# Kernel tuning notes

Measured on AMD Instinct MI355X. Metric: run time of the kernel, lower is better.

The kernel has to match this reference:

```python
import jax, jax.numpy as jnp
import numpy as np

IMAGE_SIZE = 256
PSIZE = 8
STRIDE = 4
WINDOW = IMAGE_SIZE + 1 - PSIZE  # 249


def _build_indices():
    # replicate image2patch.__init__ mask construction
    cur = np.arange(0, WINDOW, STRIDE)
    if cur[-1] != WINDOW - 1:
        cur = np.append(cur, WINDOW - 1)
    grid = np.arange(WINDOW * WINDOW).reshape(WINDOW, WINDOW)
    mask = grid[np.ix_(cur, cur)].reshape(-1)  # [M] window-origin flat indices
    rows = mask // WINDOW  # [M] patch top-left row
    cols = mask % WINDOW   # [M] patch top-left col
    k = np.arange(PSIZE * PSIZE)
    di, dj = k // PSIZE, k % PSIZE  # offsets within patch; flat index k = i*PSIZE + j
    r_full = rows[:, None] + di[None, :]  # [M, PSIZE^2]
    c_full = cols[:, None] + dj[None, :]  # [M, PSIZE^2]
    return jnp.asarray(r_full, dtype=jnp.int32), jnp.asarray(c_full, dtype=jnp.int32)

R_IDX, C_IDX = _build_indices()


def setup_inputs() -> dict:
    key = jax.random.key(0)
    x = jax.random.normal(key, (32, 8, IMAGE_SIZE, IMAGE_SIZE), dtype=jnp.float32)
    return {"input_data": x}


def reference(input_data):
    # output[b*c, m, i*PSIZE+j] = input_data[b, c, rows[m]+i, cols[m]+j]
    B, C, H, W = input_data.shape
    x = input_data.reshape(B * C, H, W)
    out = x[:, R_IDX, C_IDX]  # [B*C, M, PSIZE^2] vectorized sliding-window gather
    return out
```

## Files before the change

kernel.cpp:

```cpp
#include <hip/hip_runtime.h>


constexpr unsigned NPDIM   = 63;
constexpr unsigned PATCHES = NPDIM * NPDIM;
constexpr unsigned CHUNKS  = 16;
constexpr unsigned NIMG    = 256;

__global__ __launch_bounds__(256) void image2patch_kernel(
    const float4* __restrict__ in4, float4* __restrict__ out4) {
    unsigned gid = blockIdx.x * 256u + threadIdx.x;

    unsigned k4 = gid & 15u;
    unsigned pn = gid >> 4;
    unsigned n  = pn / PATCHES;
    unsigned p  = pn - n * PATCHES;
    unsigned pr = p / NPDIM;
    unsigned pc = p - pr * NPDIM;

    unsigned row  = pr * 4u + (k4 >> 1);
    unsigned col4 = pc + (k4 & 1u);

    out4[gid] = in4[n * 16384u + row * 64u + col4];
}

extern "C" void kernel_launch(void* const* d_in, const int* in_sizes, int n_in,
                              void* d_out, int out_size, void* d_ws, size_t ws_size,
                              hipStream_t stream) {
    const float4* in4 = (const float4*)d_in[0];
    float4* out4 = (float4*)d_out;
    unsigned total4 = NIMG * PATCHES * CHUNKS;
    unsigned blocks = total4 / 256u;
    image2patch_kernel<<<blocks, 256, 0, stream>>>(in4, out4);
}
```

Baseline: 298.5 us.

## Stage patch-row input strip in LDS and emit patches per block

Each block now handles one patch row of one image. It loads the 8x256 input strip into shared memory once, with padded rows to limit bank conflicts, then writes all 63 patches from LDS. This replaces redundant global gathers, where each input element was read about four times, with coalesced loads and LDS reads. In exchange it adds a barrier, uses only 1008 of 1024 thread slots in the write loop, and launches fewer, larger blocks.

```diff
diff --git a/kernel.cpp b/kernel.cpp
--- a/kernel.cpp
+++ b/kernel.cpp
@@ -4,23 +4,39 @@
 constexpr unsigned NPDIM   = 63;
 constexpr unsigned PATCHES = NPDIM * NPDIM;
 constexpr unsigned CHUNKS  = 16;
-constexpr unsigned NIMG    = 256;
+constexpr unsigned ROWPAD  = 65;
 
 __global__ __launch_bounds__(256) void image2patch_kernel(
     const float4* __restrict__ in4, float4* __restrict__ out4) {
-    unsigned gid = blockIdx.x * 256u + threadIdx.x;
+    __shared__ float4 lds4[8 * ROWPAD];
 
-    unsigned k4 = gid & 15u;
-    unsigned pn = gid >> 4;
-    unsigned n  = pn / PATCHES;
-    unsigned p  = pn - n * PATCHES;
-    unsigned pr = p / NPDIM;
-    unsigned pc = p - pr * NPDIM;
+    unsigned bid = blockIdx.x;
+    unsigned n   = bid / NPDIM;
+    unsigned pr  = bid - n * NPDIM;
 
-    unsigned row  = pr * 4u + (k4 >> 1);
-    unsigned col4 = pc + (k4 & 1u);
+    unsigned inbase4 = n * 16384u + pr * 256u;
+    unsigned t = threadIdx.x;
+    {
+        unsigned r0 = t >> 6, c0 = t & 63u;
+        lds4[r0 * ROWPAD + c0] = in4[inbase4 + t];
+        unsigned i1 = t + 256u;
+        unsigned r1 = i1 >> 6, c1 = i1 & 63u;
+        lds4[r1 * ROWPAD + c1] = in4[inbase4 + i1];
+    }
+    __syncthreads();
 
-    out4[gid] = in4[n * 16384u + row * 64u + col4];
+    unsigned outbase4 = (n * PATCHES + pr * NPDIM) * CHUNKS;
+    #pragma unroll
+    for (unsigned it = 0; it < 4; ++it) {
+        unsigned i = it * 256u + t;
+        if (i < NPDIM * CHUNKS) {
+            unsigned pc  = i >> 4;
+            unsigned k4  = i & 15u;
+            unsigned di  = k4 >> 1;
+            unsigned dj4 = k4 & 1u;
+            out4[outbase4 + i] = lds4[di * ROWPAD + pc + dj4];
+        }
+    }
 }
 
 extern "C" void kernel_launch(void* const* d_in, const int* in_sizes, int n_in,
@@ -28,7 +44,6 @@
                               hipStream_t stream) {
     const float4* in4 = (const float4*)d_in[0];
     float4* out4 = (float4*)d_out;
-    unsigned total4 = NIMG * PATCHES * CHUNKS;
-    unsigned blocks = total4 / 256u;
+    unsigned blocks = 256u * NPDIM;
     image2patch_kernel<<<blocks, 256, 0, stream>>>(in4, out4);
 }
```

Result: no change. 298.2 us (-0.1%).
